# Kernel optimization log

Measured on AMD Instinct MI355X. Metric: run time of the kernel, lower is better.

## Reference

```python
import jax, jax.numpy as jnp
import numpy as np

B, S, E, H = 2, 1024, 1024, 16
Dh = E // H


def setup_inputs() -> dict:
    key = jax.random.key(0)
    ks = jax.random.split(key, 32)
    sc = 1.0 / np.sqrt(E)  # xavier-ish scale
    inp = {}
    names_x = ["x_q_a", "x_q_b", "x_kv_a", "x_kv_b"]
    for i, n in enumerate(names_x):
        inp[n] = jax.random.normal(ks[i], (B, S, E), jnp.float32)
    # causal mask, broadcastable to (B, H, S, S); masked where == 0
    inp["mask"] = jnp.tril(jnp.ones((S, S), jnp.int32))[None, None, :, :]
    inp["layer_theta"] = jnp.float32(0.3)
    inp["thetas_head"] = 0.1 * jax.random.normal(ks[4], (H,), jnp.float32)
    i = 5
    for p in ["q", "k", "v", "o"]:
        inp[p + "_wa"] = sc * jax.random.normal(ks[i], (E, E), jnp.float32); i += 1
        inp[p + "_wb"] = sc * jax.random.normal(ks[i], (E, E), jnp.float32); i += 1
        inp[p + "_ba"] = jnp.zeros((E,), jnp.float32)
        inp[p + "_bb"] = jnp.zeros((E,), jnp.float32)
    return inp


def _qc_dense(xa, xb, wa, wb, ba, bb, j2):
    # F.linear: x @ W.T + b ; j2 is a scalar so (Wb*j2) factors out
    out_a = xa @ wa.T + ba + (xb @ wb.T) * j2
    out_b = xa @ wb.T + bb + xb @ wa.T
    return out_a, out_b


def _shape(x):
    # (B,S,E) -> (B,H,S,Dh)
    return x.reshape(B, S, H, Dh).transpose(0, 2, 1, 3)


def _unshape(x):
    return x.transpose(0, 2, 1, 3).reshape(B, S, E)


def _rope(x):
    # standard rotate-half RoPE on last dim, positions over axis -2
    inv_freq = 1.0 / (10000.0 ** (jnp.arange(0, Dh, 2, dtype=jnp.float32) / Dh))
    ang = jnp.arange(S, dtype=jnp.float32)[:, None] * inv_freq[None, :]  # (S, Dh/2)
    cos = jnp.concatenate([jnp.cos(ang), jnp.cos(ang)], axis=-1)  # (S, Dh)
    sin = jnp.concatenate([jnp.sin(ang), jnp.sin(ang)], axis=-1)
    x1, x2 = x[..., : Dh // 2], x[..., Dh // 2:]
    rot = jnp.concatenate([-x2, x1], axis=-1)
    return x * cos + rot * sin


def reference(x_q_a, x_q_b, x_kv_a, x_kv_b, mask, layer_theta, thetas_head,
              q_wa, q_wb, q_ba, q_bb, k_wa, k_wb, k_ba, k_bb,
              v_wa, v_wb, v_ba, v_bb, o_wa, o_wb, o_ba, o_bb):
    j2 = jnp.sin(2.0 * layer_theta) - 1.0
    qa, qb = _qc_dense(x_q_a, x_q_b, q_wa, q_wb, q_ba, q_bb, j2)
    ka, kb = _qc_dense(x_kv_a, x_kv_b, k_wa, k_wb, k_ba, k_bb, j2)
    va, vb = _qc_dense(x_kv_a, x_kv_b, v_wa, v_wb, v_ba, v_bb, j2)
    qa, qb = _rope(_shape(qa)), _rope(_shape(qb))
    ka, kb = _rope(_shape(ka)), _rope(_shape(kb))
    va, vb = _shape(va), _shape(vb)
    j2h = (jnp.sin(2.0 * thetas_head) - 1.0).reshape(1, H, 1, 1)
    # dual QC score matrices (B,H,S,S)
    s_a = jnp.einsum("bhqd,bhkd->bhqk", qa, ka) + jnp.einsum("bhqd,bhkd->bhqk", qb, kb) * j2h
    s_b = jnp.einsum("bhqd,bhkd->bhqk", qa, kb) + jnp.einsum("bhqd,bhkd->bhqk", qb, ka)
    mag = jnp.sqrt(s_a * s_a + s_b * s_b + 1e-8) / np.sqrt(Dh)
    mag = jnp.where(mask == 0, -1e9, mag)
    attn = jax.nn.softmax(mag, axis=-1)
    out_a = _unshape(jnp.einsum("bhqk,bhkd->bhqd", attn, va))
    out_b = _unshape(jnp.einsum("bhqk,bhkd->bhqd", attn, vb))
    return _qc_dense(out_a, out_b, o_wa, o_wb, o_ba, o_bb, j2)
```

## Files before the change

### kernel.cpp

```cpp
#include <hip/hip_runtime.h>
#include <math.h>
#include <stdint.h>

#define BATCH 2
#define SEQ   1024
#define EMB   1024
#define NH    16
#define DH    64
#define BSE   (BATCH*SEQ*EMB)
#define MROWS (BATCH*SEQ)

typedef unsigned short u16;
typedef __attribute__((ext_vector_type(8))) short short8;
typedef __attribute__((ext_vector_type(4))) float f32x4;

__device__ __forceinline__ float bf2f(u16 u) {
    return __uint_as_float(((unsigned int)u) << 16);
}
__device__ __forceinline__ u16 f2bf(float f) {
    unsigned int x = __float_as_uint(f);
    x += 0x7FFFu + ((x >> 16) & 1u);
    return (u16)(x >> 16);
}

__device__ __forceinline__ void async_copy16(const void* g, void* l) {
    __builtin_amdgcn_global_load_lds(
        (const __attribute__((address_space(1))) unsigned int*)g,
        (__attribute__((address_space(3))) unsigned int*)l,
        16, 0, 0);
}

struct PackArgs {
    const float* src[20];
    u16*         dst[20];
    int          scaled[20];
};

__global__ __launch_bounds__(256) void pack_kernel(PackArgs pa, const float* __restrict__ theta)
{
    const int e = blockIdx.y;
    const size_t i = ((size_t)blockIdx.x * 256 + threadIdx.x) * 4;
    float sc = 1.0f;
    if (pa.scaled[e]) sc = sinf(2.0f * theta[0]) - 1.0f;
    float4 v = *(const float4*)(pa.src[e] + i);
    ushort4 o;
    o.x = f2bf(v.x * sc); o.y = f2bf(v.y * sc);
    o.z = f2bf(v.z * sc); o.w = f2bf(v.w * sc);
    *(ushort4*)(pa.dst[e] + i) = o;
}

struct GemmArgs {
    const u16*   A1s[8];
    const u16*   A2s[8];
    const u16*   Blo[8];
    const u16*   Bhi[8];
    const float* bias[8];
    void*        dst[8];
    int          mode[8];
};

template<int SPLITK>
__global__ __launch_bounds__(256) void mfma_gemm(GemmArgs ga)
{
    __shared__ u16 sA[128][32];
    __shared__ u16 sB[128][32];

    const int t    = threadIdx.x;
    const int lane = t & 63;
    const int w    = t >> 6;
    const int wx   = w & 1;
    const int wy   = w >> 1;
    const int n0   = blockIdx.y * 128;
    const int m0   = blockIdx.x * 128;
    const int ko   = (SPLITK == 2) ? blockIdx.z : 0;
    const int seg  = n0 >> 10;
    const int nloc = n0 & 1023;

    const int srow = t >> 2;
    const int sb   = (t & 3) * 16;

    f32x4 acc[4][4] = {};

    const char* A1 = (const char*)ga.A1s[seg];
    const char* A2 = (const char*)ga.A2s[seg];
    const char* Bl = (const char*)ga.Blo[seg];
    const char* Bh = (const char*)ga.Bhi[seg];
    if (SPLITK == 2 && ko) { A1 = A2; Bl = Bh; }

    const int frow = lane & 15;
    const int quad = lane >> 4;

    const int NKT = (SPLITK == 2) ? 32 : 64;
    for (int kt = 0; kt < NKT; ++kt) {
        const char* As = (SPLITK == 1 && (kt & 32)) ? A2 : A1;
        const char* Bs = (SPLITK == 1 && (kt & 32)) ? Bh : Bl;
        const size_t kbyte = (size_t)(kt & 31) * 64;

        __syncthreads();
        #pragma unroll
        for (int r = 0; r < 2; ++r) {
            const int row = r*64 + srow;
            const int ldsoff = (r*64 + w*16) * 64;
            async_copy16(As + (size_t)(m0 + row)*2048 + kbyte + sb,
                         (char*)&sA[0][0] + ldsoff);
            async_copy16(Bs + (size_t)(nloc + row)*2048 + kbyte + sb,
                         (char*)&sB[0][0] + ldsoff);
        }
        __syncthreads();

        short8 af[4], bfr[4];
        #pragma unroll
        for (int i = 0; i < 4; ++i)
            af[i] = *(const short8*)&sA[wy*64 + i*16 + frow][quad*8];
        #pragma unroll
        for (int j = 0; j < 4; ++j)
            bfr[j] = *(const short8*)&sB[wx*64 + j*16 + frow][quad*8];

        #pragma unroll
        for (int i = 0; i < 4; ++i)
            #pragma unroll
            for (int j = 0; j < 4; ++j)
                acc[i][j] = __builtin_amdgcn_mfma_f32_16x16x32_bf16(
                                af[i], bfr[j], acc[i][j], 0, 0, 0);
    }

    const float* bias = ga.bias[seg];
    const int mode = ga.mode[seg];

    #pragma unroll
    for (int j = 0; j < 4; ++j) {
        const int c = nloc + wx*64 + j*16 + frow;
        const float bv = (SPLITK == 2 && ko) ? 0.0f : bias[c];
        #pragma unroll
        for (int i = 0; i < 4; ++i) {
            #pragma unroll
            for (int reg = 0; reg < 4; ++reg) {
                const int m = m0 + wy*64 + i*16 + quad*4 + reg;
                const float val = acc[i][j][reg] + bv;
                if (mode == 1) {
                    if (SPLITK == 2)
                        atomicAdd((float*)ga.dst[seg] + (size_t)m*1024 + c, val);
                    else
                        ((float*)ga.dst[seg])[(size_t)m*1024 + c] = val;
                } else if (mode == 2) {
                    ((u16*)ga.dst[seg])[((size_t)(m >> 10) << 20) + (size_t)c*1024 + (m & 1023)] = f2bf(val);
                } else {
                    ((u16*)ga.dst[seg])[(size_t)m*1024 + c] = f2bf(val);
                }
            }
        }
    }
}

__global__ __launch_bounds__(256) void rope_kernel(
    u16* qa, u16* qb, u16* ka, u16* kb)
{
    u16* p;
    switch (blockIdx.y) {
        case 0:  p = qa; break;
        case 1:  p = qb; break;
        case 2:  p = ka; break;
        default: p = kb; break;
    }
    const int i   = blockIdx.x * 256 + threadIdx.x;
    const int d   = i & 31;
    const int hh  = (i >> 5) & (NH - 1);
    const int row = i >> 9;
    const int s   = row & (SEQ - 1);
    const size_t base = (size_t)row * EMB + hh * DH;

    float x1 = bf2f(p[base + d]);
    float x2 = bf2f(p[base + d + 32]);
    const float invf_rev = expf(-(float)d * 0.28782313662425576f) * 0.15915494309189535f;
    float rev = (float)s * invf_rev;
    rev -= floorf(rev);
    const float sn = __builtin_amdgcn_sinf(rev);
    const float cs = __builtin_amdgcn_cosf(rev);
    p[base + d]      = f2bf(x1 * cs - x2 * sn);
    p[base + d + 32] = f2bf(x2 * cs + x1 * sn);
}

__global__ __launch_bounds__(256) void attn_mfma(
    const u16* __restrict__ qa, const u16* __restrict__ qb,
    const u16* __restrict__ ka, const u16* __restrict__ kb,
    const u16* __restrict__ vat, const u16* __restrict__ vbt,
    const float* __restrict__ thetas,
    u16* __restrict__ oa, u16* __restrict__ ob)
{
    __shared__ u16 sKa[64][64];
    __shared__ u16 sKb[64][64];
    __shared__ u16 sVa[64][64];
    __shared__ u16 sVb[64][64];
    __shared__ u16 sP[4][16][72];

    const int t    = threadIdx.x;
    const int lane = t & 63;
    const int w    = t >> 6;
    const int L15  = lane & 15;
    const int quad = lane >> 4;

    const int bid  = blockIdx.x;
    const int aa   = (bid >> 5) & 7;
    const int qt   = (bid >> 8) ? aa : (15 - aa);
    const int bh   = bid & 31;
    const int h    = bh & 15;
    const int b    = bh >> 4;

    const float j2h = sinf(2.0f * thetas[h]) - 1.0f;

    const int   qrow  = qt*64 + w*16 + L15;
    const size_t qbase = (size_t)(b*SEQ + qrow) * EMB + h*DH;
    short8 fqa[2], fqb[2], fjqb[2];
    fqa[0] = *(const short8*)(qa + qbase + quad*8);
    fqa[1] = *(const short8*)(qa + qbase + 32 + quad*8);
    fqb[0] = *(const short8*)(qb + qbase + quad*8);
    fqb[1] = *(const short8*)(qb + qbase + 32 + quad*8);
    #pragma unroll
    for (int s2 = 0; s2 < 2; ++s2) {
        short8 src = fqb[s2], dst;
        #pragma unroll
        for (int j = 0; j < 8; ++j)
            dst[j] = (short)f2bf(bf2f((u16)src[j]) * j2h);
        fjqb[s2] = dst;
    }

    f32x4 acc_a[4] = {};
    f32x4 acc_b[4] = {};
    float l_lane[4] = {0.f, 0.f, 0.f, 0.f};

    const int subrow = lane >> 3;
    const int g      = (lane & 7) ^ subrow;
    const int swz    = L15 & 7;

    for (int kt = 0; kt <= qt; ++kt) {
        __syncthreads();
        #pragma unroll
        for (int i = 0; i < 2; ++i) {
            const int row = w*16 + i*8 + subrow;
            const int ldsoff = (w*16 + i*8) * 128;
            const size_t ktok = (size_t)(b*SEQ + kt*64 + row);
            async_copy16((const char*)ka + ktok*2048 + h*128 + g*16,
                         (char*)&sKa[0][0] + ldsoff);
            async_copy16((const char*)kb + ktok*2048 + h*128 + g*16,
                         (char*)&sKb[0][0] + ldsoff);
            const size_t vrow = (size_t)b*1048576 + (size_t)(h*64 + row)*1024 + kt*64;
            async_copy16((const char*)vat + vrow*2 + g*16,
                         (char*)&sVa[0][0] + ldsoff);
            async_copy16((const char*)vbt + vrow*2 + g*16,
                         (char*)&sVb[0][0] + ldsoff);
        }
        __syncthreads();

        f32x4 sa[4] = {}, sb[4] = {};
        #pragma unroll
        for (int n = 0; n < 4; ++n) {
            const u16* rKa = &sKa[n*16 + L15][0];
            const u16* rKb = &sKb[n*16 + L15][0];
            short8 ka0 = *(const short8*)(rKa + (( quad      ^ swz) << 3));
            short8 ka1 = *(const short8*)(rKa + (((4 + quad) ^ swz) << 3));
            short8 kb0 = *(const short8*)(rKb + (( quad      ^ swz) << 3));
            short8 kb1 = *(const short8*)(rKb + (((4 + quad) ^ swz) << 3));
            sa[n] = __builtin_amdgcn_mfma_f32_16x16x32_bf16(fqa[0],  ka0, sa[n], 0, 0, 0);
            sa[n] = __builtin_amdgcn_mfma_f32_16x16x32_bf16(fqa[1],  ka1, sa[n], 0, 0, 0);
            sa[n] = __builtin_amdgcn_mfma_f32_16x16x32_bf16(fjqb[0], kb0, sa[n], 0, 0, 0);
            sa[n] = __builtin_amdgcn_mfma_f32_16x16x32_bf16(fjqb[1], kb1, sa[n], 0, 0, 0);
            sb[n] = __builtin_amdgcn_mfma_f32_16x16x32_bf16(fqa[0],  kb0, sb[n], 0, 0, 0);
            sb[n] = __builtin_amdgcn_mfma_f32_16x16x32_bf16(fqa[1],  kb1, sb[n], 0, 0, 0);
            sb[n] = __builtin_amdgcn_mfma_f32_16x16x32_bf16(fqb[0],  ka0, sb[n], 0, 0, 0);
            sb[n] = __builtin_amdgcn_mfma_f32_16x16x32_bf16(fqb[1],  ka1, sb[n], 0, 0, 0);
        }

        float p[4][4];
        if (kt == qt) {
            #pragma unroll
            for (int n = 0; n < 4; ++n)
                #pragma unroll
                for (int r = 0; r < 4; ++r) {
                    const float A = sa[n][r], B = sb[n][r];
                    const float mag = __builtin_amdgcn_sqrtf(A*A + B*B + 1e-8f) * 0.125f;
                    const bool masked = (n*16 + L15) > (w*16 + quad*4 + r);
                    p[n][r] = masked ? 0.0f
                                     : __builtin_amdgcn_exp2f(mag * 1.44269504f);
                }
        } else {
            #pragma unroll
            for (int n = 0; n < 4; ++n)
                #pragma unroll
                for (int r = 0; r < 4; ++r) {
                    const float A = sa[n][r], B = sb[n][r];
                    const float mag = __builtin_amdgcn_sqrtf(A*A + B*B + 1e-8f) * 0.125f;
                    p[n][r] = __builtin_amdgcn_exp2f(mag * 1.44269504f);
                }
        }
        #pragma unroll
        for (int r = 0; r < 4; ++r)
            l_lane[r] += (p[0][r] + p[1][r]) + (p[2][r] + p[3][r]);

        #pragma unroll
        for (int n = 0; n < 4; ++n)
            #pragma unroll
            for (int r = 0; r < 4; ++r)
                sP[w][quad*4 + r][n*16 + L15] = f2bf(p[n][r]);

        short8 pf0 = *(const short8*)&sP[w][L15][quad*8];
        short8 pf1 = *(const short8*)&sP[w][L15][32 + quad*8];

        #pragma unroll
        for (int n = 0; n < 4; ++n) {
            const u16* rVa = &sVa[n*16 + L15][0];
            const u16* rVb = &sVb[n*16 + L15][0];
            short8 va0 = *(const short8*)(rVa + (( quad      ^ swz) << 3));
            short8 va1 = *(const short8*)(rVa + (((4 + quad) ^ swz) << 3));
            short8 vb0 = *(const short8*)(rVb + (( quad      ^ swz) << 3));
            short8 vb1 = *(const short8*)(rVb + (((4 + quad) ^ swz) << 3));
            acc_a[n] = __builtin_amdgcn_mfma_f32_16x16x32_bf16(pf0, va0, acc_a[n], 0, 0, 0);
            acc_a[n] = __builtin_amdgcn_mfma_f32_16x16x32_bf16(pf1, va1, acc_a[n], 0, 0, 0);
            acc_b[n] = __builtin_amdgcn_mfma_f32_16x16x32_bf16(pf0, vb0, acc_b[n], 0, 0, 0);
            acc_b[n] = __builtin_amdgcn_mfma_f32_16x16x32_bf16(pf1, vb1, acc_b[n], 0, 0, 0);
        }
    }

    float inv[4];
    #pragma unroll
    for (int r = 0; r < 4; ++r) {
        float l = l_lane[r];
        #pragma unroll
        for (int off = 8; off >= 1; off >>= 1)
            l += __shfl_xor(l, off, 64);
        inv[r] = 1.0f / l;
    }

    #pragma unroll
    for (int reg = 0; reg < 4; ++reg) {
        const size_t tok = (size_t)(b*SEQ + qt*64 + w*16 + quad*4 + reg);
        #pragma unroll
        for (int n = 0; n < 4; ++n) {
            const size_t idx = tok*EMB + h*DH + n*16 + L15;
            oa[idx] = f2bf(acc_a[n][reg] * inv[reg]);
            ob[idx] = f2bf(acc_b[n][reg] * inv[reg]);
        }
    }
}

extern "C" void kernel_launch(void* const* d_in, const int* in_sizes, int n_in,
                              void* d_out, int out_size, void* d_ws, size_t ws_size,
                              hipStream_t stream)
{
    const float* x_q_a  = (const float*)d_in[0];
    const float* x_q_b  = (const float*)d_in[1];
    const float* x_kv_a = (const float*)d_in[2];
    const float* x_kv_b = (const float*)d_in[3];
    const float* theta    = (const float*)d_in[5];
    const float* thetas_h = (const float*)d_in[6];
    const float* q_wa = (const float*)d_in[7];
    const float* q_wb = (const float*)d_in[8];
    const float* q_ba = (const float*)d_in[9];
    const float* q_bb = (const float*)d_in[10];
    const float* k_wa = (const float*)d_in[11];
    const float* k_wb = (const float*)d_in[12];
    const float* k_ba = (const float*)d_in[13];
    const float* k_bb = (const float*)d_in[14];
    const float* v_wa = (const float*)d_in[15];
    const float* v_wb = (const float*)d_in[16];
    const float* v_ba = (const float*)d_in[17];
    const float* v_bb = (const float*)d_in[18];
    const float* o_wa = (const float*)d_in[19];
    const float* o_wb = (const float*)d_in[20];
    const float* o_ba = (const float*)d_in[21];
    const float* o_bb = (const float*)d_in[22];

    u16* W = (u16*)d_ws;
    const size_t XN = (size_t)BSE;
    const size_t WN = (size_t)EMB*EMB;
    u16* xq_a16  = W;
    u16* xq_b16  = W + XN;
    u16* xkv_a16 = W + 2*XN;
    u16* xkv_b16 = W + 3*XN;
    u16* wbase   = W + 4*XN;
    u16* q_wa16  = wbase;
    u16* q_wb16  = wbase + WN;
    u16* k_wa16  = wbase + 2*WN;
    u16* k_wb16  = wbase + 3*WN;
    u16* v_wa16  = wbase + 4*WN;
    u16* v_wb16  = wbase + 5*WN;
    u16* o_wa16  = wbase + 6*WN;
    u16* o_wb16  = wbase + 7*WN;
    u16* q_wbs16 = wbase + 8*WN;
    u16* k_wbs16 = wbase + 9*WN;
    u16* v_wbs16 = wbase + 10*WN;
    u16* o_wbs16 = wbase + 11*WN;
    u16* qkv     = wbase + 12*WN;
    u16* qa16 = qkv;
    u16* qb16 = qkv + XN;
    u16* ka16 = qkv + 2*XN;
    u16* kb16 = qkv + 3*XN;
    u16* vat16 = qkv + 4*XN;
    u16* vbt16 = qkv + 5*XN;
    u16* ao16 = xq_a16;
    u16* bo16 = xq_b16;

    float* out_a = (float*)d_out;
    float* out_b = out_a + (size_t)BSE;

    PackArgs pa;
    int si = 0;
    auto add = [&](const float* s, u16* d, int scaled, int chunks) {
        for (int c = 0; c < chunks; ++c) {
            pa.src[si] = s + (size_t)c * WN;
            pa.dst[si] = d + (size_t)c * WN;
            pa.scaled[si] = scaled;
            ++si;
        }
    };
    add(x_q_a,  xq_a16,  0, 2);
    add(x_q_b,  xq_b16,  0, 2);
    add(x_kv_a, xkv_a16, 0, 2);
    add(x_kv_b, xkv_b16, 0, 2);
    add(q_wa, q_wa16, 0, 1);  add(q_wb, q_wb16, 0, 1);
    add(k_wa, k_wa16, 0, 1);  add(k_wb, k_wb16, 0, 1);
    add(v_wa, v_wa16, 0, 1);  add(v_wb, v_wb16, 0, 1);
    add(o_wa, o_wa16, 0, 1);  add(o_wb, o_wb16, 0, 1);
    add(q_wb, q_wbs16, 1, 1); add(k_wb, k_wbs16, 1, 1);
    add(v_wb, v_wbs16, 1, 1); add(o_wb, o_wbs16, 1, 1);
    pack_kernel<<<dim3(WN/1024, 20), 256, 0, stream>>>(pa, theta);

    hipMemsetAsync(d_out, 0, (size_t)out_size * sizeof(float), stream);

    GemmArgs g12;
    const u16* a1s[6] = { xq_a16, xq_a16, xkv_a16, xkv_a16, xkv_a16, xkv_a16 };
    const u16* a2s[6] = { xq_b16, xq_b16, xkv_b16, xkv_b16, xkv_b16, xkv_b16 };
    const u16* blo[6] = { q_wa16, q_wb16, k_wa16, k_wb16, v_wa16, v_wb16 };
    const u16* bhi[6] = { q_wbs16, q_wa16, k_wbs16, k_wa16, v_wbs16, v_wa16 };
    const float* bia[6] = { q_ba, q_bb, k_ba, k_bb, v_ba, v_bb };
    void* dsts[6] = { qa16, qb16, ka16, kb16, vat16, vbt16 };
    const int modes[6] = { 0, 0, 0, 0, 2, 2 };
    for (int s = 0; s < 6; ++s) {
        g12.A1s[s] = a1s[s]; g12.A2s[s] = a2s[s];
        g12.Blo[s] = blo[s]; g12.Bhi[s] = bhi[s];
        g12.bias[s] = bia[s]; g12.dst[s] = dsts[s]; g12.mode[s] = modes[s];
    }
    for (int s = 6; s < 8; ++s) {
        g12.A1s[s] = a1s[0]; g12.A2s[s] = a2s[0];
        g12.Blo[s] = blo[0]; g12.Bhi[s] = bhi[0];
        g12.bias[s] = bia[0]; g12.dst[s] = dsts[0]; g12.mode[s] = 0;
    }
    mfma_gemm<1><<<dim3(MROWS/128, 48), 256, 0, stream>>>(g12);

    rope_kernel<<<dim3((BATCH*SEQ*NH*32)/256, 4), 256, 0, stream>>>(qa16, qb16, ka16, kb16);

    attn_mfma<<<BATCH*NH*(SEQ/64), 256, 0, stream>>>(qa16, qb16, ka16, kb16,
                                                     vat16, vbt16, thetas_h, ao16, bo16);

    GemmArgs g3;
    for (int s = 0; s < 8; ++s) {
        g3.A1s[s] = ao16; g3.A2s[s] = bo16;
        g3.Blo[s] = o_wa16; g3.Bhi[s] = o_wbs16;
        g3.bias[s] = o_ba; g3.dst[s] = out_a; g3.mode[s] = 1;
    }
    g3.Blo[1] = o_wb16; g3.Bhi[1] = o_wa16; g3.bias[1] = o_bb; g3.dst[1] = out_b;
    mfma_gemm<2><<<dim3(MROWS/128, 16, 2), 256, 0, stream>>>(g3);
}
```

Baseline: 314.7 us.

## Load attention K/V fragments directly from global and split output GEMM four ways

Result: slower. 378.3 us (+20.2%).

```diff
diff --git a/kernel.cpp b/kernel.cpp
--- a/kernel.cpp
+++ b/kernel.cpp
@@ -72,7 +72,7 @@
     const int wy   = w >> 1;
     const int n0   = blockIdx.y * 128;
     const int m0   = blockIdx.x * 128;
-    const int ko   = (SPLITK == 2) ? blockIdx.z : 0;
+    const int ko   = (SPLITK >= 2) ? blockIdx.z : 0;
     const int seg  = n0 >> 10;
     const int nloc = n0 & 1023;
 
@@ -85,13 +85,15 @@
     const char* A2 = (const char*)ga.A2s[seg];
     const char* Bl = (const char*)ga.Blo[seg];
     const char* Bh = (const char*)ga.Bhi[seg];
-    if (SPLITK == 2 && ko) { A1 = A2; Bl = Bh; }
+    if (SPLITK == 2 && ko)        { A1 = A2; Bl = Bh; }
+    if (SPLITK == 4 && (ko >> 1)) { A1 = A2; Bl = Bh; }
 
     const int frow = lane & 15;
     const int quad = lane >> 4;
 
-    const int NKT = (SPLITK == 2) ? 32 : 64;
-    for (int kt = 0; kt < NKT; ++kt) {
+    const int NKT = (SPLITK == 4) ? 16 : (SPLITK == 2) ? 32 : 64;
+    const int KT0 = (SPLITK == 4) ? (ko & 1) * 16 : 0;
+    for (int kt = KT0; kt < KT0 + NKT; ++kt) {
         const char* As = (SPLITK == 1 && (kt & 32)) ? A2 : A1;
         const char* Bs = (SPLITK == 1 && (kt & 32)) ? Bh : Bl;
         const size_t kbyte = (size_t)(kt & 31) * 64;
@@ -130,7 +132,7 @@
     #pragma unroll
     for (int j = 0; j < 4; ++j) {
         const int c = nloc + wx*64 + j*16 + frow;
-        const float bv = (SPLITK == 2 && ko) ? 0.0f : bias[c];
+        const float bv = (SPLITK >= 2 && ko) ? 0.0f : bias[c];
         #pragma unroll
         for (int i = 0; i < 4; ++i) {
             #pragma unroll
@@ -138,7 +140,7 @@
                 const int m = m0 + wy*64 + i*16 + quad*4 + reg;
                 const float val = acc[i][j][reg] + bv;
                 if (mode == 1) {
-                    if (SPLITK == 2)
+                    if (SPLITK >= 2)
                         atomicAdd((float*)ga.dst[seg] + (size_t)m*1024 + c, val);
                     else
                         ((float*)ga.dst[seg])[(size_t)m*1024 + c] = val;
@@ -187,10 +189,6 @@
     const float* __restrict__ thetas,
     u16* __restrict__ oa, u16* __restrict__ ob)
 {
-    __shared__ u16 sKa[64][64];
-    __shared__ u16 sKb[64][64];
-    __shared__ u16 sVa[64][64];
-    __shared__ u16 sVb[64][64];
     __shared__ u16 sP[4][16][72];
 
     const int t    = threadIdx.x;
@@ -228,38 +226,17 @@
     f32x4 acc_b[4] = {};
     float l_lane[4] = {0.f, 0.f, 0.f, 0.f};
 
-    const int subrow = lane >> 3;
-    const int g      = (lane & 7) ^ subrow;
-    const int swz    = L15 & 7;
-
     for (int kt = 0; kt <= qt; ++kt) {
-        __syncthreads();
-        #pragma unroll
-        for (int i = 0; i < 2; ++i) {
-            const int row = w*16 + i*8 + subrow;
-            const int ldsoff = (w*16 + i*8) * 128;
-            const size_t ktok = (size_t)(b*SEQ + kt*64 + row);
-            async_copy16((const char*)ka + ktok*2048 + h*128 + g*16,
-                         (char*)&sKa[0][0] + ldsoff);
-            async_copy16((const char*)kb + ktok*2048 + h*128 + g*16,
-                         (char*)&sKb[0][0] + ldsoff);
-            const size_t vrow = (size_t)b*1048576 + (size_t)(h*64 + row)*1024 + kt*64;
-            async_copy16((const char*)vat + vrow*2 + g*16,
-                         (char*)&sVa[0][0] + ldsoff);
-            async_copy16((const char*)vbt + vrow*2 + g*16,
-                         (char*)&sVb[0][0] + ldsoff);
-        }
-        __syncthreads();
-
         f32x4 sa[4] = {}, sb[4] = {};
         #pragma unroll
         for (int n = 0; n < 4; ++n) {
-            const u16* rKa = &sKa[n*16 + L15][0];
-            const u16* rKb = &sKb[n*16 + L15][0];
-            short8 ka0 = *(const short8*)(rKa + (( quad      ^ swz) << 3));
-            short8 ka1 = *(const short8*)(rKa + (((4 + quad) ^ swz) << 3));
-            short8 kb0 = *(const short8*)(rKb + (( quad      ^ swz) << 3));
-            short8 kb1 = *(const short8*)(rKb + (((4 + quad) ^ swz) << 3));
+            const size_t tok = (size_t)(b*SEQ + kt*64 + n*16 + L15);
+            const u16* pKa = ka + tok*EMB + h*DH;
+            const u16* pKb = kb + tok*EMB + h*DH;
+            short8 ka0 = *(const short8*)(pKa + quad*8);
+            short8 ka1 = *(const short8*)(pKa + 32 + quad*8);
+            short8 kb0 = *(const short8*)(pKb + quad*8);
+            short8 kb1 = *(const short8*)(pKb + 32 + quad*8);
             sa[n] = __builtin_amdgcn_mfma_f32_16x16x32_bf16(fqa[0],  ka0, sa[n], 0, 0, 0);
             sa[n] = __builtin_amdgcn_mfma_f32_16x16x32_bf16(fqa[1],  ka1, sa[n], 0, 0, 0);
             sa[n] = __builtin_amdgcn_mfma_f32_16x16x32_bf16(fjqb[0], kb0, sa[n], 0, 0, 0);
@@ -307,12 +284,11 @@
 
         #pragma unroll
         for (int n = 0; n < 4; ++n) {
-            const u16* rVa = &sVa[n*16 + L15][0];
-            const u16* rVb = &sVb[n*16 + L15][0];
-            short8 va0 = *(const short8*)(rVa + (( quad      ^ swz) << 3));
-            short8 va1 = *(const short8*)(rVa + (((4 + quad) ^ swz) << 3));
-            short8 vb0 = *(const short8*)(rVb + (( quad      ^ swz) << 3));
-            short8 vb1 = *(const short8*)(rVb + (((4 + quad) ^ swz) << 3));
+            const size_t vrow = (size_t)b*1048576 + (size_t)(h*64 + n*16 + L15)*1024 + kt*64;
+            short8 va0 = *(const short8*)(vat + vrow + quad*8);
+            short8 va1 = *(const short8*)(vat + vrow + 32 + quad*8);
+            short8 vb0 = *(const short8*)(vbt + vrow + quad*8);
+            short8 vb1 = *(const short8*)(vbt + vrow + 32 + quad*8);
             acc_a[n] = __builtin_amdgcn_mfma_f32_16x16x32_bf16(pf0, va0, acc_a[n], 0, 0, 0);
             acc_a[n] = __builtin_amdgcn_mfma_f32_16x16x32_bf16(pf1, va1, acc_a[n], 0, 0, 0);
             acc_b[n] = __builtin_amdgcn_mfma_f32_16x16x32_bf16(pf0, vb0, acc_b[n], 0, 0, 0);
@@ -458,5 +434,5 @@
         g3.bias[s] = o_ba; g3.dst[s] = out_a; g3.mode[s] = 1;
     }
     g3.Blo[1] = o_wb16; g3.Bhi[1] = o_wa16; g3.bias[1] = o_bb; g3.dst[1] = out_b;
-    mfma_gemm<2><<<dim3(MROWS/128, 16, 2), 256, 0, stream>>>(g3);
-}
+    mfma_gemm<4><<<dim3(MROWS/128, 16, 4), 256, 0, stream>>>(g3);
+}
```
